# Kernel optimization log

Measured on AMD Instinct MI355X. Metric: run time of the kernel, lower is better.

The kernel has to match this reference:

```python
import jax, jax.numpy as jnp
import numpy as np

B, D, F, T, H = 256, 128, 8, 128, 128


def setup_inputs() -> dict:
    key = jax.random.key(0)
    ks = jax.random.split(key, 6)
    inp = jax.random.normal(ks[0], (B, D, F, T), jnp.float32)
    # encode_attn: Linear(F*T + 2*H -> 1); weight laid out as [hidden | cell | x]
    w_attn = jax.random.normal(ks[1], (F * T + 2 * H,), jnp.float32) * 0.02
    b_attn = jax.random.normal(ks[2], (), jnp.float32) * 0.02
    # LSTM (single layer), PyTorch gate order i, f, g, o
    W_ih = jax.random.normal(ks[3], (4 * H, D * F), jnp.float32) * 0.02
    W_hh = jax.random.normal(ks[4], (4 * H, H), jnp.float32) * 0.02
    b_ih = jax.random.normal(ks[5], (4 * H,), jnp.float32) * 0.02
    b_hh = jnp.zeros((4 * H,), jnp.float32)
    return {"input": inp, "w_attn": w_attn, "b_attn": b_attn,
            "W_ih": W_ih, "W_hh": W_hh, "b_ih": b_ih, "b_hh": b_hh}


def reference(input, w_attn, b_attn, W_ih, W_hh, b_ih, b_hh):
    Bd, Dd, Fd, Td = input.shape
    Hd = W_hh.shape[1]
    # split attention weight per cat order: (hidden_state, cell_state, x)
    w_h = w_attn[:Hd]
    w_c = w_attn[Hd:2 * Hd]
    w_x = w_attn[2 * Hd:]
    x_flat = input.reshape(Bd, Dd, Fd * Td)           # [B, D, F*T]
    ex = x_flat @ w_x                                  # [B, D], constant over t
    xs = jnp.moveaxis(input, 3, 0)                     # [T, B, D, F]

    def step(carry, x_t):
        h, c = carry                                   # [B, H] each
        # attention logits: h/c contributions are per-batch scalars broadcast over drives
        e = ex + (h @ w_h + c @ w_c + b_attn)[:, None]  # [B, D]
        a = jax.nn.softmax(e, axis=-1)                 # softmax over drives
        x_hat = (a[:, :, None] * x_t).reshape(Bd, Dd * Fd)  # [B, D*F]
        gates = x_hat @ W_ih.T + h @ W_hh.T + b_ih + b_hh   # [B, 4H]
        i, f, g, o = jnp.split(gates, 4, axis=-1)
        c_new = jax.nn.sigmoid(f) * c + jax.nn.sigmoid(i) * jnp.tanh(g)
        h_new = jax.nn.sigmoid(o) * jnp.tanh(c_new)
        return (h_new, c_new), h_new

    h0 = jnp.zeros((Bd, Hd), input.dtype)
    c0 = jnp.zeros((Bd, Hd), input.dtype)
    _, hs = jax.lax.scan(step, (h0, c0), xs)           # hs: [T, B, H]
    return jnp.transpose(hs, (1, 0, 2))                # [B, T, H] == hidden_states[:, 1:]
```

## Files before the change

### kernel.cpp

```cpp
#include <hip/hip_runtime.h>
#include <cstdint>
#include <cstddef>

#define Bn 256
#define Dn 128
#define Fn 8
#define Tn 128
#define Hn 128
#define Kn 1024
#define Mn 512

typedef float f32x4 __attribute__((ext_vector_type(4)));
typedef short s16x8 __attribute__((ext_vector_type(8)));
typedef _Float16 h16x2 __attribute__((ext_vector_type(2)));
typedef _Float16 h16x8 __attribute__((ext_vector_type(8)));

#if defined(__has_builtin)
#if __has_builtin(__builtin_amdgcn_cvt_pkrtz)
#define HAVE_PKRTZ 1
#else
#define HAVE_PKRTZ 0
#endif
#else
#define HAVE_PKRTZ 0
#endif

__device__ __forceinline__ uint32_t pack2_f16(float a, float b) {
#if HAVE_PKRTZ
  typedef __fp16 fp16x2_t __attribute__((ext_vector_type(2)));
  union { fp16x2_t v; uint32_t u; } cv;
  cv.v = __builtin_amdgcn_cvt_pkrtz(a, b);
  return cv.u;
#else
  union { h16x2 h; uint32_t u; } cv;
  cv.h.x = (_Float16)a; cv.h.y = (_Float16)b;
  return cv.u;
#endif
}
__device__ __forceinline__ float sigm(float x) { return 1.0f / (1.0f + __expf(-x)); }
__device__ __forceinline__ float tanh_fast(float x) { return 1.0f - 2.0f / (__expf(2.0f * x) + 1.0f); }

__global__ __launch_bounds__(256) void k_ex(const float* __restrict__ input,
                                            const float* __restrict__ w_attn,
                                            float* __restrict__ ex) {
  __shared__ float wx[Kn];
  const int tid = threadIdx.x;
  ((float4*)wx)[tid] = ((const float4*)(w_attn + 2 * Hn))[tid];
  __syncthreads();
  const int w = tid >> 6, lane = tid & 63;
  const int gid = blockIdx.x * 4 + w;
  const float4* xp = (const float4*)(input + (size_t)gid * Kn);
  const float4* wx4 = (const float4*)wx;
  float acc = 0.f;
#pragma unroll
  for (int r = 0; r < 4; ++r) {
    float4 x = xp[lane + r * 64];
    float4 ww = wx4[lane + r * 64];
    acc += x.x * ww.x + x.y * ww.y + x.z * ww.z + x.w * ww.w;
  }
#pragma unroll
  for (int off = 32; off; off >>= 1) acc += __shfl_xor(acc, off);
  if (lane == 0) ex[gid] = acc;
}

__global__ __launch_bounds__(256) void k_prep(const float* __restrict__ W_ih,
                                              const float* __restrict__ W_hh,
                                              unsigned short* __restrict__ whf,
                                              unsigned short* __restrict__ whh) {
  const int bid = blockIdx.x;
  const int tid = threadIdx.x;
  if (bid < 256) {
    const int gid = bid * 256 + tid;
    const int lane = gid & 63;
    const int kt = (gid >> 6) & 31;
    const int mt = gid >> 11;
    const int row = mt * 16 + (lane & 15);
    const int col = kt * 32 + (lane >> 4) * 8;
    const float* src = W_ih + row * Kn + col;
    uint4 ph;
    ph.x = pack2_f16(src[0], src[1]);
    ph.y = pack2_f16(src[2], src[3]);
    ph.z = pack2_f16(src[4], src[5]);
    ph.w = pack2_f16(src[6], src[7]);
    ((uint4*)whf)[gid] = ph;
  } else {
    const int g = (bid - 256) * 256 + tid;
    const int l = g & 63;
    const int kf = (g >> 6) & 3;
    const int nt = g >> 8;
    const int row = nt * 16 + (l & 15);
    const int col = kf * 32 + (l >> 4) * 8;
    const float* src = W_hh + (size_t)row * Hn + col;
    uint4 ph;
    ph.x = pack2_f16(src[0], src[1]);
    ph.y = pack2_f16(src[2], src[3]);
    ph.z = pack2_f16(src[4], src[5]);
    ph.w = pack2_f16(src[6], src[7]);
    ((uint4*)whh)[g] = ph;
  }
}

__global__ __launch_bounds__(256, 2) void k_gates(
    const float* __restrict__ input, const float* __restrict__ ex,
    const unsigned short* __restrict__ whf,
    unsigned short* __restrict__ gx) {
  __shared__ __align__(16) unsigned char smem[34816];
  __shared__ float a_lds[Dn];
  __shared__ float sred[8];
  unsigned short* buf0 = (unsigned short*)smem;
  unsigned short* buf1 = buf0 + 8192;
  _Float16* lds_out = (_Float16*)smem;

  const int tid = threadIdx.x;
  const int bid = blockIdx.x;
  const int p = (bid >> 3) & 3;
  const int b = (bid & 7) | ((bid >> 5) << 3);
  const int w = tid >> 6;
  const int lane = tid & 63;
  const int quad = lane >> 4;
  const int l15 = lane & 15;

  float v = (tid < Dn) ? ex[b * Dn + tid] : -3.4e38f;
  float m = v;
#pragma unroll
  for (int off = 32; off; off >>= 1) m = fmaxf(m, __shfl_xor(m, off));
  if (lane == 0) sred[w] = m;
  __syncthreads();
  m = fmaxf(fmaxf(sred[0], sred[1]), fmaxf(sred[2], sred[3]));
  float e = (tid < Dn) ? __expf(v - m) : 0.f;
  float s = e;
#pragma unroll
  for (int off = 32; off; off >>= 1) s += __shfl_xor(s, off);
  if (lane == 0) sred[4 + w] = s;
  __syncthreads();
  s = sred[4] + sred[5] + sred[6] + sred[7];
  if (tid < Dn) a_lds[tid] = e / s;

  f32x4 acc[2][8];
#pragma unroll
  for (int i = 0; i < 2; ++i)
#pragma unroll
    for (int j = 0; j < 8; ++j) { f32x4 z = {0.f, 0.f, 0.f, 0.f}; acc[i][j] = z; }

  const float* xb = input + (size_t)b * Kn * Tn;
  const int mtg0 = p * 8 + w * 2;

  h16x8 wcur[4], wnxt[4];
#pragma unroll
  for (int mt = 0; mt < 2; ++mt)
#pragma unroll
    for (int kf = 0; kf < 2; ++kf) {
      const size_t fo = (((size_t)(mtg0 + mt) * 32 + kf) * 64 + lane) * 8;
      wcur[mt * 2 + kf] = *(const h16x8*)(whf + fo);
    }

  __syncthreads();

  float xr[2][2][8];
#pragma unroll
  for (int ck = 0; ck < 2; ++ck)
#pragma unroll
    for (int ct = 0; ct < 2; ++ct) {
      const int kb = 2 * w + ck;
      const float* col = xb + (size_t)(kb * 8) * Tn + lane + 64 * ct;
#pragma unroll
      for (int j = 0; j < 8; ++j) xr[ck][ct][j] = col[(size_t)j * Tn];
    }
#pragma unroll
  for (int ck = 0; ck < 2; ++ck) {
    const int kb = 2 * w + ck;
    const float av = a_lds[kb];
#pragma unroll
    for (int ct = 0; ct < 2; ++ct) {
      const int tt = lane + 64 * ct;
      uint4 pk;
      pk.x = pack2_f16(av * xr[ck][ct][0], av * xr[ck][ct][1]);
      pk.y = pack2_f16(av * xr[ck][ct][2], av * xr[ck][ct][3]);
      pk.z = pack2_f16(av * xr[ck][ct][4], av * xr[ck][ct][5]);
      pk.w = pack2_f16(av * xr[ck][ct][6], av * xr[ck][ct][7]);
      *(uint4*)(buf0 + (size_t)(kb * 128 + tt) * 8) = pk;
    }
  }
  __syncthreads();

  for (int kt = 0; kt < 16; ++kt) {
    unsigned short* cur = (kt & 1) ? buf1 : buf0;
    unsigned short* nxt = (kt & 1) ? buf0 : buf1;
    if (kt < 15) {
      const int k0n = (kt + 1) * 64;
#pragma unroll
      for (int ck = 0; ck < 2; ++ck)
#pragma unroll
        for (int ct = 0; ct < 2; ++ct) {
          const int kb = 2 * w + ck;
          const float* col = xb + (size_t)(k0n + kb * 8) * Tn + lane + 64 * ct;
#pragma unroll
          for (int j = 0; j < 8; ++j) xr[ck][ct][j] = col[(size_t)j * Tn];
        }
#pragma unroll
      for (int mt = 0; mt < 2; ++mt)
#pragma unroll
        for (int kf = 0; kf < 2; ++kf) {
          const size_t fo = (((size_t)(mtg0 + mt) * 32 + (kt + 1) * 2 + kf) * 64 + lane) * 8;
          wnxt[mt * 2 + kf] = *(const h16x8*)(whf + fo);
        }
    }
#pragma unroll
    for (int kf = 0; kf < 2; ++kf) {
      h16x8 bfr[8];
      const int kbr = kf * 4 + quad;
#pragma unroll
      for (int nt = 0; nt < 8; ++nt)
        bfr[nt] = *(const h16x8*)(cur + (size_t)(kbr * 128 + nt * 16 + l15) * 8);
#pragma unroll
      for (int mt = 0; mt < 2; ++mt)
#pragma unroll
        for (int nt = 0; nt < 8; ++nt) {
          acc[mt][nt] = __builtin_amdgcn_mfma_f32_16x16x32_f16(wcur[mt * 2 + kf], bfr[nt], acc[mt][nt], 0, 0, 0);
        }
    }
    if (kt < 15) {
#pragma unroll
      for (int ck = 0; ck < 2; ++ck) {
        const int kb = 2 * w + ck;
        const float av = a_lds[(kt + 1) * 8 + kb];
#pragma unroll
        for (int ct = 0; ct < 2; ++ct) {
          const int tt = lane + 64 * ct;
          uint4 pk;
          pk.x = pack2_f16(av * xr[ck][ct][0], av * xr[ck][ct][1]);
          pk.y = pack2_f16(av * xr[ck][ct][2], av * xr[ck][ct][3]);
          pk.z = pack2_f16(av * xr[ck][ct][4], av * xr[ck][ct][5]);
          pk.w = pack2_f16(av * xr[ck][ct][6], av * xr[ck][ct][7]);
          *(uint4*)(nxt + (size_t)(kb * 128 + tt) * 8) = pk;
        }
      }
#pragma unroll
      for (int i = 0; i < 4; ++i) wcur[i] = wnxt[i];
    }
    __syncthreads();
  }

#pragma unroll
  for (int mt = 0; mt < 2; ++mt)
#pragma unroll
    for (int nt = 0; nt < 8; ++nt)
#pragma unroll
      for (int r = 0; r < 4; ++r) {
        const int jl = (w * 2 + mt) * 16 + quad * 4 + r;
        lds_out[jl * 136 + nt * 16 + l15] = (_Float16)acc[mt][nt][r];
      }
  __syncthreads();
  {
    const int jr = tid >> 1, half = tid & 1;
    const uint4* lsrc = (const uint4*)(lds_out + jr * 136 + half * 64);
    uint4* gdst = (uint4*)(gx + ((size_t)(b * Mn + p * 128 + jr)) * Tn + half * 64);
#pragma unroll
    for (int i = 0; i < 8; ++i) gdst[i] = lsrc[i];
  }
}

__global__ __launch_bounds__(256, 1) void k_rec(
    const unsigned short* __restrict__ gx, const unsigned short* __restrict__ whh,
    const float* __restrict__ b_ih, const float* __restrict__ b_hh,
    float* __restrict__ out) {
  __shared__ unsigned short gxl[512 * 130];
  __shared__ __align__(16) _Float16 h2l[2][Hn];

  const int tid = threadIdx.x;
  const int b = blockIdx.x;

  {
    const uint4* src = (const uint4*)(gx + (size_t)b * Mn * Tn);
#pragma unroll
    for (int it = 0; it < 32; ++it) {
      const int c = it * 256 + tid;
      const int row = c >> 4, off = c & 15;
      uint4 vv = src[c];
      uint32_t* dst = (uint32_t*)((char*)gxl + (size_t)row * 260 + off * 16);
      dst[0] = vv.x; dst[1] = vv.y; dst[2] = vv.z; dst[3] = vv.w;
    }
  }
  const int w = tid >> 6, l = tid & 63;
  const bool lo = (l < 32);
  const int d = w * 32 + (l & 31);
  const int j0 = d + (lo ? 0 : 128);
  const int j1 = j0 + 256;
  const float bs0 = b_ih[j0] + b_hh[j0];
  const float bs1 = b_ih[j1] + b_hh[j1];

  h16x8 wf[8][4];
#pragma unroll
  for (int ntl = 0; ntl < 8; ++ntl) {
    const int nt = (ntl >> 1) * 8 + 2 * w + (ntl & 1);
#pragma unroll
    for (int kf = 0; kf < 4; ++kf) {
      const size_t fo = (((size_t)nt * 4 + kf) * 64 + l) * 8;
      wf[ntl][kf] = *(const h16x8*)(whh + fo);
    }
  }
  if (tid < Hn) h2l[0][tid] = (_Float16)0.f;
  float c_st = 0.f;
  __syncthreads();

  float* outp = out + (size_t)b * Tn * Hn;
  const int aoff = (l >> 4) * 8;
  for (int t = 0; t < Tn; ++t) {
    const float g0 = bs0 + (float)(*(const _Float16*)&gxl[j0 * 130 + t]);
    const float g1 = bs1 + (float)(*(const _Float16*)&gxl[j1 * 130 + t]);
    const _Float16* hb = &h2l[t & 1][0];
    h16x8 af0 = *(const h16x8*)(hb + 0 * 32 + aoff);
    h16x8 af1 = *(const h16x8*)(hb + 1 * 32 + aoff);
    h16x8 af2 = *(const h16x8*)(hb + 2 * 32 + aoff);
    h16x8 af3 = *(const h16x8*)(hb + 3 * 32 + aoff);
    f32x4 acc[8];
#pragma unroll
    for (int ntl = 0; ntl < 8; ++ntl) {
      f32x4 z = {0.f, 0.f, 0.f, 0.f};
      z = __builtin_amdgcn_mfma_f32_16x16x32_f16(af0, wf[ntl][0], z, 0, 0, 0);
      z = __builtin_amdgcn_mfma_f32_16x16x32_f16(af1, wf[ntl][1], z, 0, 0, 0);
      z = __builtin_amdgcn_mfma_f32_16x16x32_f16(af2, wf[ntl][2], z, 0, 0, 0);
      z = __builtin_amdgcn_mfma_f32_16x16x32_f16(af3, wf[ntl][3], z, 0, 0, 0);
      acc[ntl] = z;
    }
    const float va = (l < 16) ? acc[0][0] : (l < 32) ? acc[1][0]
                   : (l < 48) ? acc[2][0] : acc[3][0];
    const float vb = (l < 16) ? acc[4][0] : (l < 32) ? acc[5][0]
                   : (l < 48) ? acc[6][0] : acc[7][0];
    const float a = va + g0;
    const float bb = vb + g1;
    const float aX = __shfl_xor(a, 32);
    const float bX = __shfl_xor(bb, 32);
    const float gi = lo ? a : aX;
    const float gf = lo ? aX : a;
    const float gg = lo ? bb : bX;
    const float go = lo ? bX : bb;
    c_st = sigm(gf) * c_st + sigm(gi) * tanh_fast(gg);
    const float hnew = sigm(go) * tanh_fast(c_st);
    if (lo) {
      outp[t * Hn + d] = hnew;
      h2l[(t + 1) & 1][d] = (_Float16)hnew;
    }
    __syncthreads();
  }
}

extern "C" void kernel_launch(void* const* d_in, const int* in_sizes, int n_in,
                              void* d_out, int out_size, void* d_ws, size_t ws_size,
                              hipStream_t stream) {
  (void)in_sizes; (void)n_in; (void)out_size; (void)ws_size;
  const float* input = (const float*)d_in[0];
  const float* w_attn = (const float*)d_in[1];
  const float* W_ih = (const float*)d_in[3];
  const float* W_hh = (const float*)d_in[4];
  const float* b_ih = (const float*)d_in[5];
  const float* b_hh = (const float*)d_in[6];
  float* out = (float*)d_out;

  char* ws = (char*)d_ws;
  float* ex = (float*)ws;
  unsigned short* whf = (unsigned short*)(ws + 131072);
  unsigned short* whh = (unsigned short*)(ws + 1179648);
  unsigned short* gxw = (unsigned short*)(ws + 1310720);

  k_ex<<<8192, 256, 0, stream>>>(input, w_attn, ex);
  k_prep<<<288, 256, 0, stream>>>(W_ih, W_hh, whf, whh);
  k_gates<<<1024, 256, 0, stream>>>(input, ex, whf, gxw);
  k_rec<<<Bn, 256, 0, stream>>>(gxw, whh, b_ih, b_hh, out);
}
```

Measured before the change: 341.6 us.

## Widen recurrent kernel to 512 threads, transpose gx layout, merge prep kernels

```diff
diff --git a/kernel.cpp b/kernel.cpp
--- a/kernel.cpp
+++ b/kernel.cpp
@@ -11,8 +11,8 @@
 #define Mn 512
 
 typedef float f32x4 __attribute__((ext_vector_type(4)));
-typedef short s16x8 __attribute__((ext_vector_type(8)));
 typedef _Float16 h16x2 __attribute__((ext_vector_type(2)));
+typedef _Float16 h16x4 __attribute__((ext_vector_type(4)));
 typedef _Float16 h16x8 __attribute__((ext_vector_type(8)));
 
 #if defined(__has_builtin)
@@ -40,35 +40,33 @@
 __device__ __forceinline__ float sigm(float x) { return 1.0f / (1.0f + __expf(-x)); }
 __device__ __forceinline__ float tanh_fast(float x) { return 1.0f - 2.0f / (__expf(2.0f * x) + 1.0f); }
 
-__global__ __launch_bounds__(256) void k_ex(const float* __restrict__ input,
-                                            const float* __restrict__ w_attn,
-                                            float* __restrict__ ex) {
+__global__ __launch_bounds__(256) void k_ex_prep(
+    const float* __restrict__ input, const float* __restrict__ w_attn,
+    const float* __restrict__ W_ih, const float* __restrict__ W_hh,
+    float* __restrict__ ex, unsigned short* __restrict__ whf,
+    unsigned short* __restrict__ whh) {
   __shared__ float wx[Kn];
   const int tid = threadIdx.x;
-  ((float4*)wx)[tid] = ((const float4*)(w_attn + 2 * Hn))[tid];
-  __syncthreads();
-  const int w = tid >> 6, lane = tid & 63;
-  const int gid = blockIdx.x * 4 + w;
-  const float4* xp = (const float4*)(input + (size_t)gid * Kn);
-  const float4* wx4 = (const float4*)wx;
-  float acc = 0.f;
-#pragma unroll
-  for (int r = 0; r < 4; ++r) {
-    float4 x = xp[lane + r * 64];
-    float4 ww = wx4[lane + r * 64];
-    acc += x.x * ww.x + x.y * ww.y + x.z * ww.z + x.w * ww.w;
-  }
-#pragma unroll
-  for (int off = 32; off; off >>= 1) acc += __shfl_xor(acc, off);
-  if (lane == 0) ex[gid] = acc;
-}
-
-__global__ __launch_bounds__(256) void k_prep(const float* __restrict__ W_ih,
-                                              const float* __restrict__ W_hh,
-                                              unsigned short* __restrict__ whf,
-                                              unsigned short* __restrict__ whh) {
-  const int bid = blockIdx.x;
-  const int tid = threadIdx.x;
+  if (blockIdx.x < 8192) {
+    ((float4*)wx)[tid] = ((const float4*)(w_attn + 2 * Hn))[tid];
+    __syncthreads();
+    const int w = tid >> 6, lane = tid & 63;
+    const int gid = blockIdx.x * 4 + w;
+    const float4* xp = (const float4*)(input + (size_t)gid * Kn);
+    const float4* wx4 = (const float4*)wx;
+    float acc = 0.f;
+#pragma unroll
+    for (int r = 0; r < 4; ++r) {
+      float4 x = xp[lane + r * 64];
+      float4 ww = wx4[lane + r * 64];
+      acc += x.x * ww.x + x.y * ww.y + x.z * ww.z + x.w * ww.w;
+    }
+#pragma unroll
+    for (int off = 32; off; off >>= 1) acc += __shfl_xor(acc, off);
+    if (lane == 0) ex[gid] = acc;
+    return;
+  }
+  const int bid = blockIdx.x - 8192;
   if (bid < 256) {
     const int gid = bid * 256 + tid;
     const int lane = gid & 63;
@@ -244,103 +242,96 @@
 #pragma unroll
   for (int mt = 0; mt < 2; ++mt)
 #pragma unroll
-    for (int nt = 0; nt < 8; ++nt)
-#pragma unroll
-      for (int r = 0; r < 4; ++r) {
-        const int jl = (w * 2 + mt) * 16 + quad * 4 + r;
-        lds_out[jl * 136 + nt * 16 + l15] = (_Float16)acc[mt][nt][r];
-      }
+    for (int nt = 0; nt < 8; ++nt) {
+      const int jl = (w * 2 + mt) * 16 + quad * 4;
+      const int tt = nt * 16 + l15;
+      h16x4 v4;
+      v4.x = (_Float16)acc[mt][nt][0];
+      v4.y = (_Float16)acc[mt][nt][1];
+      v4.z = (_Float16)acc[mt][nt][2];
+      v4.w = (_Float16)acc[mt][nt][3];
+      *(h16x4*)(lds_out + tt * 136 + jl) = v4;
+    }
   __syncthreads();
   {
-    const int jr = tid >> 1, half = tid & 1;
-    const uint4* lsrc = (const uint4*)(lds_out + jr * 136 + half * 64);
-    uint4* gdst = (uint4*)(gx + ((size_t)(b * Mn + p * 128 + jr)) * Tn + half * 64);
+    const int tr = tid >> 1, half = tid & 1;
+    const uint4* lsrc = (const uint4*)(lds_out + tr * 136 + half * 64);
+    uint4* gdst = (uint4*)(gx + (((size_t)b * Tn + tr) * Mn) + p * 128 + half * 64);
 #pragma unroll
     for (int i = 0; i < 8; ++i) gdst[i] = lsrc[i];
   }
 }
 
-__global__ __launch_bounds__(256, 1) void k_rec(
+__global__ __launch_bounds__(512) void k_rec(
     const unsigned short* __restrict__ gx, const unsigned short* __restrict__ whh,
     const float* __restrict__ b_ih, const float* __restrict__ b_hh,
     float* __restrict__ out) {
-  __shared__ unsigned short gxl[512 * 130];
   __shared__ __align__(16) _Float16 h2l[2][Hn];
 
   const int tid = threadIdx.x;
   const int b = blockIdx.x;
-
-  {
-    const uint4* src = (const uint4*)(gx + (size_t)b * Mn * Tn);
-#pragma unroll
-    for (int it = 0; it < 32; ++it) {
-      const int c = it * 256 + tid;
-      const int row = c >> 4, off = c & 15;
-      uint4 vv = src[c];
-      uint32_t* dst = (uint32_t*)((char*)gxl + (size_t)row * 260 + off * 16);
-      dst[0] = vv.x; dst[1] = vv.y; dst[2] = vv.z; dst[3] = vv.w;
-    }
-  }
   const int w = tid >> 6, l = tid & 63;
-  const bool lo = (l < 32);
-  const int d = w * 32 + (l & 31);
-  const int j0 = d + (lo ? 0 : 128);
-  const int j1 = j0 + 256;
-  const float bs0 = b_ih[j0] + b_hh[j0];
-  const float bs1 = b_ih[j1] + b_hh[j1];
-
-  h16x8 wf[8][4];
-#pragma unroll
-  for (int ntl = 0; ntl < 8; ++ntl) {
-    const int nt = (ntl >> 1) * 8 + 2 * w + (ntl & 1);
+  const int d = w * 16 + (l & 15);
+
+  float bs[4];
+#pragma unroll
+  for (int q = 0; q < 4; ++q) bs[q] = b_ih[q * 128 + d] + b_hh[q * 128 + d];
+
+  h16x8 wf[4][4];
+#pragma unroll
+  for (int q = 0; q < 4; ++q) {
+    const int nt = q * 8 + w;
 #pragma unroll
     for (int kf = 0; kf < 4; ++kf) {
       const size_t fo = (((size_t)nt * 4 + kf) * 64 + l) * 8;
-      wf[ntl][kf] = *(const h16x8*)(whh + fo);
+      wf[q][kf] = *(const h16x8*)(whh + fo);
     }
   }
   if (tid < Hn) h2l[0][tid] = (_Float16)0.f;
   float c_st = 0.f;
+
+  const unsigned short* gb = gx + (size_t)b * Tn * Mn;
+  unsigned short gc0 = gb[0 * 128 + d];
+  unsigned short gc1 = gb[1 * 128 + d];
+  unsigned short gc2 = gb[2 * 128 + d];
+  unsigned short gc3 = gb[3 * 128 + d];
   __syncthreads();
 
   float* outp = out + (size_t)b * Tn * Hn;
   const int aoff = (l >> 4) * 8;
   for (int t = 0; t < Tn; ++t) {
-    const float g0 = bs0 + (float)(*(const _Float16*)&gxl[j0 * 130 + t]);
-    const float g1 = bs1 + (float)(*(const _Float16*)&gxl[j1 * 130 + t]);
+    const int tn = (t < Tn - 1) ? t + 1 : t;
+    const unsigned short* gr = gb + (size_t)tn * Mn;
+    const unsigned short gn0 = gr[0 * 128 + d];
+    const unsigned short gn1 = gr[1 * 128 + d];
+    const unsigned short gn2 = gr[2 * 128 + d];
+    const unsigned short gn3 = gr[3 * 128 + d];
     const _Float16* hb = &h2l[t & 1][0];
-    h16x8 af0 = *(const h16x8*)(hb + 0 * 32 + aoff);
-    h16x8 af1 = *(const h16x8*)(hb + 1 * 32 + aoff);
-    h16x8 af2 = *(const h16x8*)(hb + 2 * 32 + aoff);
-    h16x8 af3 = *(const h16x8*)(hb + 3 * 32 + aoff);
-    f32x4 acc[8];
-#pragma unroll
-    for (int ntl = 0; ntl < 8; ++ntl) {
-      f32x4 z = {0.f, 0.f, 0.f, 0.f};
-      z = __builtin_amdgcn_mfma_f32_16x16x32_f16(af0, wf[ntl][0], z, 0, 0, 0);
-      z = __builtin_amdgcn_mfma_f32_16x16x32_f16(af1, wf[ntl][1], z, 0, 0, 0);
-      z = __builtin_amdgcn_mfma_f32_16x16x32_f16(af2, wf[ntl][2], z, 0, 0, 0);
-      z = __builtin_amdgcn_mfma_f32_16x16x32_f16(af3, wf[ntl][3], z, 0, 0, 0);
-      acc[ntl] = z;
-    }
-    const float va = (l < 16) ? acc[0][0] : (l < 32) ? acc[1][0]
-                   : (l < 48) ? acc[2][0] : acc[3][0];
-    const float vb = (l < 16) ? acc[4][0] : (l < 32) ? acc[5][0]
-                   : (l < 48) ? acc[6][0] : acc[7][0];
-    const float a = va + g0;
-    const float bb = vb + g1;
-    const float aX = __shfl_xor(a, 32);
-    const float bX = __shfl_xor(bb, 32);
-    const float gi = lo ? a : aX;
-    const float gf = lo ? aX : a;
-    const float gg = lo ? bb : bX;
-    const float go = lo ? bX : bb;
+    const h16x8 af0 = *(const h16x8*)(hb + 0 + aoff);
+    const h16x8 af1 = *(const h16x8*)(hb + 32 + aoff);
+    const h16x8 af2 = *(const h16x8*)(hb + 64 + aoff);
+    const h16x8 af3 = *(const h16x8*)(hb + 96 + aoff);
+    const f32x4 zzero = {0.f, 0.f, 0.f, 0.f};
+    float gt[4];
+#pragma unroll
+    for (int q = 0; q < 4; ++q) {
+      f32x4 za = __builtin_amdgcn_mfma_f32_16x16x32_f16(af0, wf[q][0], zzero, 0, 0, 0);
+      za = __builtin_amdgcn_mfma_f32_16x16x32_f16(af1, wf[q][1], za, 0, 0, 0);
+      f32x4 zb = __builtin_amdgcn_mfma_f32_16x16x32_f16(af2, wf[q][2], zzero, 0, 0, 0);
+      zb = __builtin_amdgcn_mfma_f32_16x16x32_f16(af3, wf[q][3], zb, 0, 0, 0);
+      gt[q] = za[0] + zb[0];
+    }
+    const float gi = gt[0] + bs[0] + (float)(*(const _Float16*)&gc0);
+    const float gf = gt[1] + bs[1] + (float)(*(const _Float16*)&gc1);
+    const float gg = gt[2] + bs[2] + (float)(*(const _Float16*)&gc2);
+    const float go = gt[3] + bs[3] + (float)(*(const _Float16*)&gc3);
     c_st = sigm(gf) * c_st + sigm(gi) * tanh_fast(gg);
     const float hnew = sigm(go) * tanh_fast(c_st);
-    if (lo) {
+    if (l < 16) {
       outp[t * Hn + d] = hnew;
       h2l[(t + 1) & 1][d] = (_Float16)hnew;
     }
+    gc0 = gn0; gc1 = gn1; gc2 = gn2; gc3 = gn3;
     __syncthreads();
   }
 }
@@ -363,8 +354,7 @@
   unsigned short* whh = (unsigned short*)(ws + 1179648);
   unsigned short* gxw = (unsigned short*)(ws + 1310720);
 
-  k_ex<<<8192, 256, 0, stream>>>(input, w_attn, ex);
-  k_prep<<<288, 256, 0, stream>>>(W_ih, W_hh, whf, whh);
+  k_ex_prep<<<8480, 256, 0, stream>>>(input, w_attn, W_ih, W_hh, ex, whf, whh);
   k_gates<<<1024, 256, 0, stream>>>(input, ex, whf, gxw);
-  k_rec<<<Bn, 256, 0, stream>>>(gxw, whh, b_ih, b_hh, out);
-}
+  k_rec<<<Bn, 512, 0, stream>>>(gxw, whh, b_ih, b_hh, out);
+}
```

Measured after the change: 346.2 us. About the same (+1.3%).
